# Performance work log

Measured on AMD Instinct MI355X. Metric: run time of the kernel, lower is better.

## Reference

```python
import jax, jax.numpy as jnp
import numpy as np

EPS = 1e-12  # torch F.normalize eps
REG1 = 0.5
REG2 = 0.5
ALPHA = 0.5

N, D, P = 32768, 512, 4096


def setup_inputs() -> dict:
    key = jax.random.key(0)
    k1, k2, k3, k4, k5 = jax.random.split(key, 5)
    return {
        "x": jax.random.normal(k1, (N, D), dtype=jnp.float32),
        "W": jax.random.normal(k2, (P, D), dtype=jnp.float32) * (1.0 / np.sqrt(D)),
        "recon_loss": jax.random.uniform(k3, (), dtype=jnp.float32),
        "kl_loss": jax.random.uniform(k4, (), dtype=jnp.float32),
        "mmd_loss": jax.random.uniform(k5, (), dtype=jnp.float32),
    }


def _cdist(a, b):
    # Euclidean distance matrix [A, B] via the expanded-square identity.
    a2 = jnp.sum(a * a, axis=1, keepdims=True)          # [A, 1]
    b2 = jnp.sum(b * b, axis=1, keepdims=True).T        # [1, B]
    d2 = a2 + b2 - 2.0 * (a @ b.T)
    return jnp.sqrt(jnp.maximum(d2, 0.0))


def reference(x, W, recon_loss, kl_loss, mmd_loss):
    # l2 normalize along feature dim (torch F.normalize semantics)
    nrm = jnp.maximum(jnp.linalg.norm(x, axis=1, keepdims=True), EPS)
    xn = x / nrm                                        # [N, D]
    logits = xn @ W.T                                   # prototypes(x): [N, P]
    # prototype decoding loss; cdist(W, xn) == cdist(xn, W).T, reuse one matrix
    d = _cdist(xn, W)                                   # [N, P]
    prot_loss = REG1 * jnp.mean(jnp.min(d, axis=1)) + REG2 * jnp.mean(jnp.min(d, axis=0))
    cvae_loss = recon_loss + ALPHA * kl_loss + mmd_loss
    return xn, logits, cvae_loss, prot_loss
```

## Files before the change

### kernel.cpp

```cpp
#include <hip/hip_runtime.h>

#define N_ROWS 32768
#define D_DIM  512
#define P_DIM  4096

#define OUT_LOGITS (32768LL * 512)
#define OUT_CVAE   (OUT_LOGITS + 32768LL * 4096)
#define OUT_PROT   (OUT_CVAE + 1)

typedef __attribute__((ext_vector_type(8))) short short8;
typedef __attribute__((ext_vector_type(4))) float f32x4;

__device__ __forceinline__ unsigned short f2bf(float f) {
  unsigned u = __float_as_uint(f);
  u = (u + 0x7FFFu + ((u >> 16) & 1u)) >> 16;
  return (unsigned short)u;
}

__device__ __forceinline__ void gload16(const void* g, void* l) {
  __builtin_amdgcn_global_load_lds((const __attribute__((address_space(1))) void*)g,
                                   (__attribute__((address_space(3))) void*)l,
                                   16, 0, 0);
}

template <int NORM>
__global__ __launch_bounds__(256) void prep_kernel(const float* __restrict__ in,
                                                   float* __restrict__ outf,
                                                   unsigned short* __restrict__ outb,
                                                   float* __restrict__ n2) {
  int wave = threadIdx.x >> 6, lane = threadIdx.x & 63;
  int row  = blockIdx.x * 4 + wave;
  const float* p = in + (size_t)row * D_DIM + lane * 8;
  float4 v0 = *(const float4*)p;
  float4 v1 = *(const float4*)(p + 4);
  float ss = v0.x*v0.x + v0.y*v0.y + v0.z*v0.z + v0.w*v0.w
           + v1.x*v1.x + v1.y*v1.y + v1.z*v1.z + v1.w*v1.w;
#pragma unroll
  for (int m = 1; m < 64; m <<= 1) ss += __shfl_xor(ss, m);
  if (NORM) {
    float rinv = 1.0f / fmaxf(sqrtf(ss), 1e-12f);
    v0.x *= rinv; v0.y *= rinv; v0.z *= rinv; v0.w *= rinv;
    v1.x *= rinv; v1.y *= rinv; v1.z *= rinv; v1.w *= rinv;
    f32x4* qp = (f32x4*)(outf + (size_t)row * D_DIM + lane * 8);
    f32x4 a0 = {v0.x, v0.y, v0.z, v0.w};
    f32x4 a1 = {v1.x, v1.y, v1.z, v1.w};
    __builtin_nontemporal_store(a0, qp);
    __builtin_nontemporal_store(a1, qp + 1);
  } else {
    if (lane == 0) n2[row] = ss;
  }
  uint4 b;
  b.x = (unsigned)f2bf(v0.x) | ((unsigned)f2bf(v0.y) << 16);
  b.y = (unsigned)f2bf(v0.z) | ((unsigned)f2bf(v0.w) << 16);
  b.z = (unsigned)f2bf(v1.x) | ((unsigned)f2bf(v1.y) << 16);
  b.w = (unsigned)f2bf(v1.z) | ((unsigned)f2bf(v1.w) << 16);
  int tile = row >> 7, fr = (row >> 4) & 7, r = row & 15;
  size_t dst = (size_t)(tile * 16 + (lane >> 2)) * 4096
             + (size_t)((fr * 64 + (lane & 3) * 16 + r) * 8);
  *(uint4*)(outb + dst) = b;
}

__global__ __launch_bounds__(256) void init_mins(unsigned int* __restrict__ p, int n) {
  int i = blockIdx.x * 256 + threadIdx.x;
  if (i < n) p[i] = 0x7F800000u;
}

__global__ __launch_bounds__(256, 3) void gemm_fused(
    const unsigned short* __restrict__ Wb, const unsigned short* __restrict__ Xb,
    const float* __restrict__ w2, float* __restrict__ Cout,
    unsigned int* __restrict__ rowmin_g, unsigned int* __restrict__ colmin_g) {
  __shared__ __align__(16) unsigned short SA[3][4096];
  __shared__ __align__(16) unsigned short SB[3][4096];
  __shared__ unsigned int rowmin_u[128];
  __shared__ unsigned int colmin_u[128];

  const int tid = threadIdx.x;
  const int wave = tid >> 6, lane = tid & 63;
  const int q = lane >> 4, r16 = lane & 15;
  const int ww = wave >> 1, wx = wave & 1;

  const int b = blockIdx.x;
  const int tw = (b & 7) * 4 + ((b >> 3) & 3);
  const int tx = b >> 5;
  const int w0 = tw * 128, x0 = tx * 128;

  if (tid < 128) { rowmin_u[tid] = 0x7F800000u; colmin_u[tid] = 0x7F800000u; }

  const unsigned short* Wg = Wb + (size_t)(tw * 16) * 4096;
  const unsigned short* Xg = Xb + (size_t)(tx * 16) * 4096;

  f32x4 acc[4][4];
#pragma unroll
  for (int m = 0; m < 4; ++m)
#pragma unroll
    for (int n = 0; n < 4; ++n) acc[m][n] = (f32x4){0.f, 0.f, 0.f, 0.f};

  auto stg = [&](int kt, int bu) {
#pragma unroll
    for (int i = 0; i < 2; ++i) {
      int c = (tid + 256 * i) * 8;
      gload16(Wg + (size_t)kt * 4096 + c, &SA[bu][0] + c);
      gload16(Xg + (size_t)kt * 4096 + c, &SB[bu][0] + c);
    }
  };

  stg(0, 0);
  stg(1, 1);

#pragma unroll
  for (int kt = 0; kt < 16; ++kt) {
    const int cur = kt % 3;
    if (kt < 15) { asm volatile("s_waitcnt vmcnt(4)" ::: "memory"); }
    else         { asm volatile("s_waitcnt vmcnt(0)" ::: "memory"); }
    __builtin_amdgcn_s_barrier();

    short8 af[4], bf[4];
#pragma unroll
    for (int m = 0; m < 4; ++m)
      af[m] = *(const short8*)(&SA[cur][0] + ((ww * 4 + m) * 64 + lane) * 8);
#pragma unroll
    for (int n = 0; n < 4; ++n)
      bf[n] = *(const short8*)(&SB[cur][0] + ((wx * 4 + n) * 64 + lane) * 8);
    if (kt < 14) stg(kt + 2, (kt + 2) % 3);

    __builtin_amdgcn_s_setprio(1);
#pragma unroll
    for (int m = 0; m < 4; ++m)
#pragma unroll
      for (int n = 0; n < 4; ++n)
        acc[m][n] = __builtin_amdgcn_mfma_f32_16x16x32_bf16(af[m], bf[n], acc[m][n], 0, 0, 0);
    __builtin_amdgcn_s_setprio(0);
  }

  float rmin[4];
  float cmin[4][4];
#pragma unroll
  for (int n = 0; n < 4; ++n) rmin[n] = 1e30f;
#pragma unroll
  for (int m = 0; m < 4; ++m)
#pragma unroll
    for (int j = 0; j < 4; ++j) cmin[m][j] = 1e30f;

  const float* w2p = w2 + w0 + ww * 64;
#pragma unroll
  for (int m = 0; m < 4; ++m) {
    float4 w2v = *(const float4*)(w2p + m * 16 + q * 4);
    const size_t wcol = (size_t)(w0 + ww * 64 + m * 16 + q * 4);
#pragma unroll
    for (int n = 0; n < 4; ++n) {
      f32x4 c = acc[m][n];
      int xr = x0 + wx * 64 + n * 16 + r16;
      __builtin_nontemporal_store(c, (f32x4*)&Cout[(size_t)xr * P_DIM + wcol]);
      float d0 = fmaxf(fmaf(-2.f, c[0], 1.f + w2v.x), 0.f);
      float d1 = fmaxf(fmaf(-2.f, c[1], 1.f + w2v.y), 0.f);
      float d2 = fmaxf(fmaf(-2.f, c[2], 1.f + w2v.z), 0.f);
      float d3 = fmaxf(fmaf(-2.f, c[3], 1.f + w2v.w), 0.f);
      rmin[n] = fminf(rmin[n], fminf(fminf(d0, d1), fminf(d2, d3)));
      cmin[m][0] = fminf(cmin[m][0], d0);
      cmin[m][1] = fminf(cmin[m][1], d1);
      cmin[m][2] = fminf(cmin[m][2], d2);
      cmin[m][3] = fminf(cmin[m][3], d3);
    }
  }
#pragma unroll
  for (int mask = 16; mask <= 32; mask <<= 1)
#pragma unroll
    for (int n = 0; n < 4; ++n)
      rmin[n] = fminf(rmin[n], __shfl_xor(rmin[n], mask));
  if (q == 0) {
#pragma unroll
    for (int n = 0; n < 4; ++n)
      atomicMin(&rowmin_u[wx * 64 + n * 16 + r16], __float_as_uint(rmin[n]));
  }
#pragma unroll
  for (int mask = 1; mask <= 8; mask <<= 1)
#pragma unroll
    for (int m = 0; m < 4; ++m)
#pragma unroll
      for (int j = 0; j < 4; ++j)
        cmin[m][j] = fminf(cmin[m][j], __shfl_xor(cmin[m][j], mask));
  if (r16 == 0) {
#pragma unroll
    for (int m = 0; m < 4; ++m)
#pragma unroll
      for (int j = 0; j < 4; ++j)
        atomicMin(&colmin_u[ww * 64 + m * 16 + q * 4 + j], __float_as_uint(cmin[m][j]));
  }
  __syncthreads();
  if (tid < 128) atomicMin(&rowmin_g[x0 + tid], rowmin_u[tid]);
  else           atomicMin(&colmin_g[w0 + (tid - 128)], colmin_u[tid - 128]);
}

__global__ __launch_bounds__(256) void minsqrt_sum(const unsigned int* __restrict__ mins,
                                                   float* __restrict__ out) {
  int idx = blockIdx.x * 256 + threadIdx.x;
  float s = sqrtf(__uint_as_float(mins[idx]));
#pragma unroll
  for (int mask = 1; mask < 64; mask <<= 1) s += __shfl_xor(s, mask);
  __shared__ float wsum[4];
  int wave = threadIdx.x >> 6, lane = threadIdx.x & 63;
  if (lane == 0) wsum[wave] = s;
  __syncthreads();
  if (threadIdx.x == 0) out[blockIdx.x] = wsum[0] + wsum[1] + wsum[2] + wsum[3];
}

__global__ void finalize_kernel(const float* __restrict__ rowp, const float* __restrict__ colp,
                                const float* __restrict__ recon, const float* __restrict__ kl,
                                const float* __restrict__ mmd, float* __restrict__ out) {
  int lane = threadIdx.x;
  float rs = rowp[lane] + rowp[lane + 64];
  float cs = (lane < 16) ? colp[lane] : 0.0f;
#pragma unroll
  for (int mask = 1; mask < 64; mask <<= 1) {
    rs += __shfl_xor(rs, mask);
    cs += __shfl_xor(cs, mask);
  }
  if (lane == 0) {
    out[OUT_CVAE] = recon[0] + 0.5f * kl[0] + mmd[0];
    out[OUT_PROT] = 0.5f * (rs / (float)N_ROWS) + 0.5f * (cs / (float)P_DIM);
  }
}

extern "C" void kernel_launch(void* const* d_in, const int* in_sizes, int n_in,
                              void* d_out, int out_size, void* d_ws, size_t ws_size,
                              hipStream_t stream) {
  const float* x     = (const float*)d_in[0];
  const float* W     = (const float*)d_in[1];
  const float* recon = (const float*)d_in[2];
  const float* kl    = (const float*)d_in[3];
  const float* mmd   = (const float*)d_in[4];
  float* out    = (float*)d_out;
  float* xn     = out;
  float* logits = out + OUT_LOGITS;

  char* ws = (char*)d_ws;
  unsigned short* Xbf = (unsigned short*)ws;
  unsigned short* Wbf = (unsigned short*)(ws + 33554432);
  float* w2          = (float*)(ws + 37748736);
  unsigned int* rmg  = (unsigned int*)(ws + 37765120);
  unsigned int* cmg  = (unsigned int*)(ws + 37896192);
  float* rowsums     = (float*)(ws + 37912576);
  float* colsums     = (float*)(ws + 37913088);

  init_mins<<<(32768 + 4096 + 255) / 256, 256, 0, stream>>>(rmg, 32768 + 4096);
  prep_kernel<1><<<N_ROWS / 4, 256, 0, stream>>>(x, xn, Xbf, nullptr);
  prep_kernel<0><<<P_DIM / 4, 256, 0, stream>>>(W, nullptr, Wbf, w2);
  gemm_fused<<<(N_ROWS / 128) * (P_DIM / 128), 256, 0, stream>>>(
      Wbf, Xbf, w2, logits, rmg, cmg);
  minsqrt_sum<<<N_ROWS / 256, 256, 0, stream>>>(rmg, rowsums);
  minsqrt_sum<<<P_DIM / 256, 256, 0, stream>>>(cmg, colsums);
  finalize_kernel<<<1, 64, 0, stream>>>(rowsums, colsums, recon, kl, mmd, out);
}
```

Baseline: 252.0 us.

## Load GEMM fragments directly from global memory into registers, dropping LDS staging

Replaces the triple-buffered LDS pipeline (global_load_lds plus barriers) with direct per-wave global loads of pre-swizzled bf16 fragments into registers, double-buffered across k-steps. It removes the LDS traffic and block-wide barriers, and drops the occupancy hint from launch bounds. The cost is that each fragment is now fetched from global/L2 by both waves that need it, since the two waves sharing a W or X tile no longer share one LDS copy. Register pressure also rises from holding two fragment sets.

Measured after the change: 259.2 us. 2.8% more time.

```diff
diff --git a/kernel.cpp b/kernel.cpp
--- a/kernel.cpp
+++ b/kernel.cpp
@@ -15,12 +15,6 @@
   unsigned u = __float_as_uint(f);
   u = (u + 0x7FFFu + ((u >> 16) & 1u)) >> 16;
   return (unsigned short)u;
-}
-
-__device__ __forceinline__ void gload16(const void* g, void* l) {
-  __builtin_amdgcn_global_load_lds((const __attribute__((address_space(1))) void*)g,
-                                   (__attribute__((address_space(3))) void*)l,
-                                   16, 0, 0);
 }
 
 template <int NORM>
@@ -65,12 +59,10 @@
   if (i < n) p[i] = 0x7F800000u;
 }
 
-__global__ __launch_bounds__(256, 3) void gemm_fused(
+__global__ __launch_bounds__(256) void gemm_fused(
     const unsigned short* __restrict__ Wb, const unsigned short* __restrict__ Xb,
     const float* __restrict__ w2, float* __restrict__ Cout,
     unsigned int* __restrict__ rowmin_g, unsigned int* __restrict__ colmin_g) {
-  __shared__ __align__(16) unsigned short SA[3][4096];
-  __shared__ __align__(16) unsigned short SB[3][4096];
   __shared__ unsigned int rowmin_u[128];
   __shared__ unsigned int colmin_u[128];
 
@@ -86,8 +78,8 @@
 
   if (tid < 128) { rowmin_u[tid] = 0x7F800000u; colmin_u[tid] = 0x7F800000u; }
 
-  const unsigned short* Wg = Wb + (size_t)(tw * 16) * 4096;
-  const unsigned short* Xg = Xb + (size_t)(tx * 16) * 4096;
+  const unsigned short* Wg = Wb + (size_t)tw * 65536;
+  const unsigned short* Xg = Xb + (size_t)tx * 65536;
 
   f32x4 acc[4][4];
 #pragma unroll
@@ -95,40 +87,38 @@
 #pragma unroll
     for (int n = 0; n < 4; ++n) acc[m][n] = (f32x4){0.f, 0.f, 0.f, 0.f};
 
-  auto stg = [&](int kt, int bu) {
-#pragma unroll
-    for (int i = 0; i < 2; ++i) {
-      int c = (tid + 256 * i) * 8;
-      gload16(Wg + (size_t)kt * 4096 + c, &SA[bu][0] + c);
-      gload16(Xg + (size_t)kt * 4096 + c, &SB[bu][0] + c);
+  auto ldw = [&](int kt, int m) -> short8 {
+    return *(const short8*)(Wg + kt * 4096 + ((ww * 4 + m) * 64 + lane) * 8);
+  };
+  auto ldx = [&](int kt, int n) -> short8 {
+    return *(const short8*)(Xg + kt * 4096 + ((wx * 4 + n) * 64 + lane) * 8);
+  };
+
+  short8 wa[4], xa[4], wn[4], xn_[4];
+#pragma unroll
+  for (int m = 0; m < 4; ++m) { wa[m] = ldw(0, m); xa[m] = ldx(0, m); }
+
+#pragma unroll
+  for (int kt = 0; kt < 16; kt += 2) {
+#pragma unroll
+    for (int m = 0; m < 4; ++m) { wn[m] = ldw(kt + 1, m); xn_[m] = ldx(kt + 1, m); }
+    __builtin_amdgcn_s_setprio(1);
+#pragma unroll
+    for (int m = 0; m < 4; ++m)
+#pragma unroll
+      for (int n = 0; n < 4; ++n)
+        acc[m][n] = __builtin_amdgcn_mfma_f32_16x16x32_bf16(wa[m], xa[n], acc[m][n], 0, 0, 0);
+    __builtin_amdgcn_s_setprio(0);
+    if (kt + 2 < 16) {
+#pragma unroll
+      for (int m = 0; m < 4; ++m) { wa[m] = ldw(kt + 2, m); xa[m] = ldx(kt + 2, m); }
     }
-  };
-
-  stg(0, 0);
-  stg(1, 1);
-
-#pragma unroll
-  for (int kt = 0; kt < 16; ++kt) {
-    const int cur = kt % 3;
-    if (kt < 15) { asm volatile("s_waitcnt vmcnt(4)" ::: "memory"); }
-    else         { asm volatile("s_waitcnt vmcnt(0)" ::: "memory"); }
-    __builtin_amdgcn_s_barrier();
-
-    short8 af[4], bf[4];
-#pragma unroll
-    for (int m = 0; m < 4; ++m)
-      af[m] = *(const short8*)(&SA[cur][0] + ((ww * 4 + m) * 64 + lane) * 8);
-#pragma unroll
-    for (int n = 0; n < 4; ++n)
-      bf[n] = *(const short8*)(&SB[cur][0] + ((wx * 4 + n) * 64 + lane) * 8);
-    if (kt < 14) stg(kt + 2, (kt + 2) % 3);
-
     __builtin_amdgcn_s_setprio(1);
 #pragma unroll
     for (int m = 0; m < 4; ++m)
 #pragma unroll
       for (int n = 0; n < 4; ++n)
-        acc[m][n] = __builtin_amdgcn_mfma_f32_16x16x32_bf16(af[m], bf[n], acc[m][n], 0, 0, 0);
+        acc[m][n] = __builtin_amdgcn_mfma_f32_16x16x32_bf16(wn[m], xn_[n], acc[m][n], 0, 0, 0);
     __builtin_amdgcn_s_setprio(0);
   }
 
```
